# Kernel optimization log

Hardware: AMD Instinct MI355X
Metric: run time of the kernel (lower is better)

## Reference

```python
import jax, jax.numpy as jnp
import numpy as np

HEADS = 4
DIM_HEAD = 128

def setup_inputs() -> dict:
    key = jax.random.key(0)
    k1, k2, k3, k4 = jax.random.split(key, 4)
    scale = DIM_HEAD ** -0.5
    return {
        "fmap": jax.random.normal(k1, (16, 512, 32, 32), dtype=jnp.float32),
        "w_qkv": jax.random.normal(k2, (1536, 512), dtype=jnp.float32) * 0.02,
        "height": jax.random.normal(k3, (32, DIM_HEAD), dtype=jnp.float32) * scale,
        "width": jax.random.normal(k4, (32, DIM_HEAD), dtype=jnp.float32) * scale,
    }

def reference(fmap, w_qkv, height, width):
    b, c, h, w = fmap.shape
    scale = DIM_HEAD ** -0.5
    # 1x1 conv == channel GEMM: (b, 3*heads*dim_head, h, w)
    qkv = jnp.einsum('bchw,oc->bohw', fmap, w_qkv)
    # split into q,k,v and reshape to (b, heads, seq, dim_head)
    qkv = qkv.reshape(b, 3, HEADS, DIM_HEAD, h * w)
    q, k, v = (jnp.transpose(qkv[:, i], (0, 1, 3, 2)) for i in range(3))
    # content logits
    sim = jnp.einsum('bhid,bhjd->bhij', q, k) * scale
    # absolute positional bias: emb[(x,y)] = height[x] + width[y]
    emb = (height[:, None, :] + width[None, :, :]).reshape(h * w, DIM_HEAD)
    sim = sim + jnp.einsum('bhid,jd->bhij', q, emb) * scale
    attn = jax.nn.softmax(sim, axis=-1)
    out = jnp.einsum('bhij,bhjd->bhid', attn, v)  # (b, heads, seq, d)
    out = jnp.transpose(out, (0, 1, 3, 2)).reshape(b, HEADS * DIM_HEAD, h, w)
    return out
```

## Files before the change

### kernel.cpp

```cpp
#include <hip/hip_runtime.h>
#include <math.h>

#define HEADS 4
#define DIMH  128
#define NB    16
#define CIN   512
#define SEQ   1024
#define OTOT  1536
#define KQ    (CIN / 8)

typedef __attribute__((ext_vector_type(8)))  short bf16x8;
typedef __attribute__((ext_vector_type(4)))  short bf16x4;
typedef __attribute__((ext_vector_type(4)))  float f32x4;
typedef __attribute__((ext_vector_type(16))) float f32x16;

#define MFMA16(a,b,c) __builtin_amdgcn_mfma_f32_16x16x32_bf16(a,b,c,0,0,0)
#define MFMA32(a,b,c) __builtin_amdgcn_mfma_f32_32x32x16_bf16(a,b,c,0,0,0)

__device__ __forceinline__ short f2bf(float f) {
    unsigned u = __builtin_bit_cast(unsigned, f);
    u = (u + 0x7FFFu + ((u >> 16) & 1u)) >> 16;
    return (short)u;
}
__device__ __forceinline__ unsigned pk2(float lo, float hi) {
    return __builtin_amdgcn_perm(__builtin_bit_cast(unsigned, hi),
                                 __builtin_bit_cast(unsigned, lo), 0x07060302u);
}
union PF8 { unsigned u[4]; bf16x8 v; };

__device__ __forceinline__ void gll16(const short* g, short* l) {
    __builtin_amdgcn_global_load_lds(
        (const __attribute__((address_space(1))) unsigned*)g,
        (__attribute__((address_space(3))) unsigned*)l,
        16, 0, 0);
}

__global__ __launch_bounds__(256) void convert_all(const float* __restrict__ F,
                                                   const float* __restrict__ W,
                                                   short* __restrict__ FT2,
                                                   short* __restrict__ Wb2) {
    const int kq = blockIdx.y;
    if (blockIdx.z == NB) {
        const int o = blockIdx.x * 256 + threadIdx.x;
        float4 v0 = *(const float4*)&W[(size_t)o * CIN + kq * 8];
        float4 v1 = *(const float4*)&W[(size_t)o * CIN + kq * 8 + 4];
        bf16x8 pk = { f2bf(v0.x), f2bf(v0.y), f2bf(v0.z), f2bf(v0.w),
                      f2bf(v1.x), f2bf(v1.y), f2bf(v1.z), f2bf(v1.w) };
        *(bf16x8*)&Wb2[((size_t)kq * OTOT + o) * 8] = pk;
        return;
    }
    if (blockIdx.x >= 4) return;
    const int s = blockIdx.x * 256 + threadIdx.x;
    const int b = blockIdx.z;
    const float* src = F + ((size_t)b * CIN + kq * 8) * SEQ + s;
    float v[8];
    #pragma unroll
    for (int i = 0; i < 8; ++i) v[i] = src[(size_t)i * SEQ];
    bf16x8 pk = { f2bf(v[0]), f2bf(v[1]), f2bf(v[2]), f2bf(v[3]),
                  f2bf(v[4]), f2bf(v[5]), f2bf(v[6]), f2bf(v[7]) };
    *(bf16x8*)&FT2[(((size_t)b * KQ + kq) * SEQ + s) * 8] = pk;
}

__global__ __launch_bounds__(256, 3) void qkv_gemm(
    const short* __restrict__ Wb2, const short* __restrict__ FT2,
    const float* __restrict__ height, const float* __restrict__ width,
    short* __restrict__ Qo, short* __restrict__ Kfo, short* __restrict__ Vfo)
{
    __shared__ short As[2][4 * 128 * 8];
    __shared__ short Bs[2][4 * 128 * 8];

    const int L  = blockIdx.x;
    const int x8 = L & 7, m = L >> 3;
    const int g  = x8 + 8 * (m / 12);
    const int oy = m % 12;
    const int b  = g >> 3, sx = g & 7;
    const int o0 = oy * 128, s0 = sx * 128;

    const int t = threadIdx.x, l = t & 63, w = t >> 6;
    const int quad = l >> 4, ln = l & 15;
    const int wrow = (w >> 1) * 64, wcol = (w & 1) * 64;

#define STAGE(ks, buf) { \
    _Pragma("unroll") for (int r = 0; r < 4; ++r) { \
        const int task = r * 4 + w; \
        const int p = task >> 1, hf = task & 1; \
        if (p < 4) { \
            const short* gsrc = Wb2 + (((size_t)((ks) * 4 + p) * OTOT) + o0 + hf * 64 + l) * 8; \
            gll16(gsrc, &As[buf][(p * 128 + hf * 64) * 8]); \
        } else { \
            const short* gsrc = FT2 + ((((size_t)b * KQ + (ks) * 4 + (p - 4)) * SEQ) + s0 + hf * 64 + l) * 8; \
            gll16(gsrc, &Bs[buf][((p - 4) * 128 + hf * 64) * 8]); \
        } \
    } }

    f32x4 acc[4][4] = {};

    STAGE(0, 0);
    __syncthreads();

    for (int ks = 0; ks < 16; ++ks) {
        const int cb = ks & 1;
        if (ks < 15) STAGE(ks + 1, cb ^ 1);
        const short* Ab = &As[cb][0];
        const short* Bb = &Bs[cb][0];
        bf16x8 af[4], bfr[4];
        #pragma unroll
        for (int i = 0; i < 4; ++i)
            af[i]  = *(const bf16x8*)&Ab[((size_t)quad * 128 + wrow + i * 16 + ln) * 8];
        #pragma unroll
        for (int j = 0; j < 4; ++j)
            bfr[j] = *(const bf16x8*)&Bb[((size_t)quad * 128 + wcol + j * 16 + ln) * 8];
        #pragma unroll
        for (int i = 0; i < 4; ++i)
            #pragma unroll
            for (int j = 0; j < 4; ++j)
                acc[i][j] = MFMA16(af[i], bfr[j], acc[i][j]);
        __syncthreads();
    }

    const int sec = o0 >> 9;
    const int h   = (o0 >> 7) & 3;
    const size_t bh = (size_t)b * HEADS + h;

    if (sec == 0) {
        const float qs = 0.08838834764831845f * 1.4426950408889634f;
        #pragma unroll
        for (int ti = 0; ti < 4; ++ti) {
            int d = wrow + ti * 16 + quad * 4;
            #pragma unroll
            for (int tj = 0; tj < 4; ++tj) {
                int s = s0 + wcol + tj * 16 + ln;
                f32x4 a = acc[ti][tj];
                bf16x4 pk4 = { f2bf(a[0]*qs), f2bf(a[1]*qs), f2bf(a[2]*qs), f2bf(a[3]*qs) };
                *(bf16x4*)&Qo[(bh * SEQ + s) * DIMH + d] = pk4;
            }
        }
    } else if (sec == 1) {
        #pragma unroll
        for (int ti = 0; ti < 4; ++ti) {
            int d = wrow + ti * 16 + quad * 4;
            #pragma unroll
            for (int tj = 0; tj < 4; ++tj) {
                int s = s0 + wcol + tj * 16 + ln;
                float4 hv = *(const float4*)&height[(size_t)(s >> 5) * DIMH + d];
                float4 wv = *(const float4*)&width[(size_t)(s & 31) * DIMH + d];
                f32x4 a = acc[ti][tj];
                bf16x4 pk4 = { f2bf(a[0] + hv.x + wv.x), f2bf(a[1] + hv.y + wv.y),
                               f2bf(a[2] + hv.z + wv.z), f2bf(a[3] + hv.w + wv.w) };
                *(bf16x4*)&Kfo[(((size_t)bh * 16 + (d >> 3)) * SEQ + s) * 8 + (d & 7)] = pk4;
            }
        }
    } else {
        const int slot = ((ln >> 2) & 1) * 8 + (ln & 3) + ((ln >> 3) << 2);
        #pragma unroll
        for (int ti = 0; ti < 4; ++ti) {
            int d = wrow + ti * 16 + quad * 4;
            #pragma unroll
            for (int tj = 0; tj < 4; ++tj) {
                int s = s0 + wcol + tj * 16 + ln;
                size_t vb = (((size_t)bh * 64 + (s >> 4)) * DIMH) * 16 + slot;
                f32x4 a = acc[ti][tj];
                #pragma unroll
                for (int r = 0; r < 4; ++r)
                    Vfo[vb + (size_t)(d + r) * 16] = f2bf(a[r]);
            }
        }
    }
}

#define BQ 128
#define BJ 64
#define KSTR 136

#define ATTN_ITER(ti, DO_QK, DO_PRE, DO_BAR)                                        \
{                                                                                   \
    const int rd = (((ti) + 1) & 1) * (BJ * KSTR);                                  \
    const int wr = ((ti) & 1) * (BJ * KSTR);                                        \
    const short* vp0 = Vlane + (size_t)((ti) * 4) * (DIMH * 16);                    \
    bf16x8 vr[4][4];                                                                \
    _Pragma("unroll") for (int gi = 0; gi < 2; ++gi)                                \
      _Pragma("unroll") for (int dc = 0; dc < 4; ++dc)                              \
        vr[gi][dc] = *(const bf16x8*)(vp0 + (size_t)gi * (DIMH * 16) + dc * 32 * 16);\
    int4 kreg[4];                                                                   \
    if (DO_PRE) {                                                                   \
        _Pragma("unroll") for (int p = 0; p < 4; ++p)                               \
            kreg[p] = *(const int4*)(Kg + ((size_t)(p * 4 + w) * SEQ + ((ti) + 2) * BJ + l) * 8); \
    }                                                                               \
    PF8 pf[4];                                                                      \
    _Pragma("unroll") for (int g = 0; g < 4; ++g) {                                 \
        const f32x16& Sh = (g & 2) ? S1 : S0;                                       \
        const int kk = g & 1;                                                       \
        _Pragma("unroll") for (int mm = 0; mm < 4; ++mm) {                          \
            float ea = __builtin_amdgcn_exp2f(Sh[kk * 8 + 2 * mm]);                 \
            float eb = __builtin_amdgcn_exp2f(Sh[kk * 8 + 2 * mm + 1]);             \
            psum += ea + eb;                                                        \
            pf[g].u[mm] = pk2(ea, eb);                                              \
        }                                                                           \
    }                                                                               \
    _Pragma("unroll") for (int gi = 2; gi < 4; ++gi)                                \
      _Pragma("unroll") for (int dc = 0; dc < 4; ++dc)                              \
        vr[gi][dc] = *(const bf16x8*)(vp0 + (size_t)gi * (DIMH * 16) + dc * 32 * 16);\
    if (DO_QK) {                                                                    \
        S0 = (f32x16){}; S1 = (f32x16){};                                           \
        _Pragma("unroll") for (int kc = 0; kc < 8; ++kc) {                          \
            bf16x8 k0 = *(const bf16x8*)&Ks[rd + c31 * KSTR + kc * 16 + h * 8];     \
            bf16x8 k1 = *(const bf16x8*)&Ks[rd + (32 + c31) * KSTR + kc * 16 + h * 8]; \
            S0 = MFMA32(k0, qf[kc], S0);                                            \
            S1 = MFMA32(k1, qf[kc], S1);                                            \
        }                                                                           \
    }                                                                               \
    _Pragma("unroll") for (int g = 0; g < 4; ++g)                                   \
        _Pragma("unroll") for (int dc = 0; dc < 4; ++dc)                            \
            O[dc] = MFMA32(vr[g][dc], pf[g].v, O[dc]);                              \
    if (DO_PRE) {                                                                   \
        _Pragma("unroll") for (int p = 0; p < 4; ++p)                               \
            *(int4*)&Ks[wr + l * KSTR + (p * 4 + w) * 8] = kreg[p];                 \
    }                                                                               \
    if (DO_BAR) __syncthreads();                                                    \
}

__global__ __launch_bounds__(256, 2) void attn(
    const short* __restrict__ Q, const short* __restrict__ Kf,
    const short* __restrict__ Vf, float* __restrict__ out)
{
    __shared__ short Ks[2 * BJ * KSTR];

    const int t = threadIdx.x, l = t & 63, w = t >> 6;
    const int h = l >> 5, c31 = l & 31;

    const int L = blockIdx.x;
    const int x = L & 7, inner = L >> 3;
    const int bh = x * 8 + (inner >> 3);
    const int q0 = (inner & 7) * BQ;
    const size_t obase = (size_t)bh * DIMH * SEQ;

    bf16x8 qf[8];
    {
        const short* Qp = Q + ((size_t)bh * SEQ + (q0 + w * 32 + c31)) * DIMH + h * 8;
        #pragma unroll
        for (int kc = 0; kc < 8; ++kc)
            qf[kc] = *(const bf16x8*)(Qp + kc * 16);
    }

    const short* Kg = Kf + (size_t)bh * 16 * SEQ * 8;
    const short* Vlane = Vf + (size_t)bh * 64 * (DIMH * 16) + (c31 * 16 + h * 8);

    f32x16 O[4] = {};
    float psum = 0.f;

    {
        int4 k0[4], k1[4];
        #pragma unroll
        for (int p = 0; p < 4; ++p) {
            k0[p] = *(const int4*)(Kg + ((size_t)(p * 4 + w) * SEQ + l) * 8);
            k1[p] = *(const int4*)(Kg + ((size_t)(p * 4 + w) * SEQ + BJ + l) * 8);
        }
        #pragma unroll
        for (int p = 0; p < 4; ++p) {
            *(int4*)&Ks[l * KSTR + (p * 4 + w) * 8] = k0[p];
            *(int4*)&Ks[BJ * KSTR + l * KSTR + (p * 4 + w) * 8] = k1[p];
        }
    }
    __syncthreads();

    f32x16 S0 = {}, S1 = {};
    #pragma unroll
    for (int kc = 0; kc < 8; ++kc) {
        bf16x8 k0 = *(const bf16x8*)&Ks[c31 * KSTR + kc * 16 + h * 8];
        bf16x8 k1 = *(const bf16x8*)&Ks[(32 + c31) * KSTR + kc * 16 + h * 8];
        S0 = MFMA32(k0, qf[kc], S0);
        S1 = MFMA32(k1, qf[kc], S1);
    }
    __syncthreads();

    for (int p = 0; p < 7; ++p) {
        const int t0 = 2 * p;
        ATTN_ITER(t0,     true, true, true);
        ATTN_ITER(t0 + 1, true, true, true);
    }
    ATTN_ITER(14, true,  false, false);
    ATTN_ITER(15, false, false, false);

    psum += __shfl_xor(psum, 32);
    float linv = 1.0f / psum;

    #pragma unroll
    for (int dc = 0; dc < 4; ++dc)
        #pragma unroll
        for (int r = 0; r < 16; ++r) {
            int d = dc * 32 + (r & 3) + 8 * (r >> 2) + 4 * h;
            out[obase + (size_t)d * SEQ + q0 + w * 32 + c31] = O[dc][r] * linv;
        }
}

extern "C" void kernel_launch(void* const* d_in, const int* in_sizes, int n_in,
                              void* d_out, int out_size, void* d_ws, size_t ws_size,
                              hipStream_t stream) {
    const float* fmap   = (const float*)d_in[0];
    const float* w_qkv  = (const float*)d_in[1];
    const float* height = (const float*)d_in[2];
    const float* width  = (const float*)d_in[3];
    float* outp = (float*)d_out;

    const size_t n_ft  = (size_t)NB * SEQ * CIN;
    const size_t n_w   = (size_t)OTOT * CIN;
    const size_t n_qkv = (size_t)NB * HEADS * SEQ * DIMH;

    short* FT2 = (short*)d_ws;
    short* Wb2 = FT2 + n_ft;
    short* Qb  = Wb2 + n_w;
    short* Kfb = Qb + n_qkv;
    short* Vfb = Kfb + n_qkv;

    convert_all<<<dim3(6, KQ, NB + 1), 256, 0, stream>>>(fmap, w_qkv, FT2, Wb2);
    qkv_gemm<<<dim3(8 * 12 * NB), 256, 0, stream>>>(
        Wb2, FT2, height, width, Qb, Kfb, Vfb);
    attn<<<dim3(NB * HEADS * (SEQ / BQ)), 256, 0, stream>>>(Qb, Kfb, Vfb, outp);
}
```

Baseline: 171.4 us.

## Load K fragments directly from global into registers, drop LDS staging and barriers

K tiles are no longer staged through shared memory with double buffering and block barriers. Each wave instead loads its K MFMA operands straight from global memory into registers, one tile ahead, and MFMA sections are wrapped in s_setprio to raise wave priority. This removes the LDS round trip and the __syncthreads in every iteration. In exchange, every wave fetches K redundantly (four times more global/L2 traffic), register pressure rises with 16 extra bf16x8 fragments, and the loop is now fully unrolled.

```diff
diff --git a/kernel.cpp b/kernel.cpp
--- a/kernel.cpp
+++ b/kernel.cpp
@@ -170,22 +170,21 @@
 
 #define BQ 128
 #define BJ 64
-#define KSTR 136
-
-#define ATTN_ITER(ti, DO_QK, DO_PRE, DO_BAR)                                        \
+
+#define KLOAD(tile) { \
+    const short* kp = Kg + ((size_t)h * SEQ + (tile) * BJ + c31) * 8; \
+    _Pragma("unroll") for (int kc = 0; kc < 8; ++kc) { \
+        ka0[kc] = *(const bf16x8*)(kp + (size_t)(kc * 2) * SEQ * 8); \
+        ka1[kc] = *(const bf16x8*)(kp + ((size_t)(kc * 2) * SEQ + 32) * 8); \
+    } }
+
+#define ATTN_ITER(ti, DO_QK, DO_PRE)                                                \
 {                                                                                   \
-    const int rd = (((ti) + 1) & 1) * (BJ * KSTR);                                  \
-    const int wr = ((ti) & 1) * (BJ * KSTR);                                        \
     const short* vp0 = Vlane + (size_t)((ti) * 4) * (DIMH * 16);                    \
     bf16x8 vr[4][4];                                                                \
     _Pragma("unroll") for (int gi = 0; gi < 2; ++gi)                                \
       _Pragma("unroll") for (int dc = 0; dc < 4; ++dc)                              \
         vr[gi][dc] = *(const bf16x8*)(vp0 + (size_t)gi * (DIMH * 16) + dc * 32 * 16);\
-    int4 kreg[4];                                                                   \
-    if (DO_PRE) {                                                                   \
-        _Pragma("unroll") for (int p = 0; p < 4; ++p)                               \
-            kreg[p] = *(const int4*)(Kg + ((size_t)(p * 4 + w) * SEQ + ((ti) + 2) * BJ + l) * 8); \
-    }                                                                               \
     PF8 pf[4];                                                                      \
     _Pragma("unroll") for (int g = 0; g < 4; ++g) {                                 \
         const f32x16& Sh = (g & 2) ? S1 : S0;                                       \
@@ -197,34 +196,30 @@
             pf[g].u[mm] = pk2(ea, eb);                                              \
         }                                                                           \
     }                                                                               \
+    if (DO_QK) {                                                                    \
+        S0 = (f32x16){}; S1 = (f32x16){};                                           \
+        __builtin_amdgcn_s_setprio(1);                                              \
+        _Pragma("unroll") for (int kc = 0; kc < 8; ++kc) {                          \
+            S0 = MFMA32(ka0[kc], qf[kc], S0);                                       \
+            S1 = MFMA32(ka1[kc], qf[kc], S1);                                       \
+        }                                                                           \
+        __builtin_amdgcn_s_setprio(0);                                              \
+    }                                                                               \
+    if (DO_PRE) KLOAD((ti) + 2);                                                    \
     _Pragma("unroll") for (int gi = 2; gi < 4; ++gi)                                \
       _Pragma("unroll") for (int dc = 0; dc < 4; ++dc)                              \
         vr[gi][dc] = *(const bf16x8*)(vp0 + (size_t)gi * (DIMH * 16) + dc * 32 * 16);\
-    if (DO_QK) {                                                                    \
-        S0 = (f32x16){}; S1 = (f32x16){};                                           \
-        _Pragma("unroll") for (int kc = 0; kc < 8; ++kc) {                          \
-            bf16x8 k0 = *(const bf16x8*)&Ks[rd + c31 * KSTR + kc * 16 + h * 8];     \
-            bf16x8 k1 = *(const bf16x8*)&Ks[rd + (32 + c31) * KSTR + kc * 16 + h * 8]; \
-            S0 = MFMA32(k0, qf[kc], S0);                                            \
-            S1 = MFMA32(k1, qf[kc], S1);                                            \
-        }                                                                           \
-    }                                                                               \
+    __builtin_amdgcn_s_setprio(1);                                                  \
     _Pragma("unroll") for (int g = 0; g < 4; ++g)                                   \
         _Pragma("unroll") for (int dc = 0; dc < 4; ++dc)                            \
             O[dc] = MFMA32(vr[g][dc], pf[g].v, O[dc]);                              \
-    if (DO_PRE) {                                                                   \
-        _Pragma("unroll") for (int p = 0; p < 4; ++p)                               \
-            *(int4*)&Ks[wr + l * KSTR + (p * 4 + w) * 8] = kreg[p];                 \
-    }                                                                               \
-    if (DO_BAR) __syncthreads();                                                    \
+    __builtin_amdgcn_s_setprio(0);                                                  \
 }
 
 __global__ __launch_bounds__(256, 2) void attn(
     const short* __restrict__ Q, const short* __restrict__ Kf,
     const short* __restrict__ Vf, float* __restrict__ out)
 {
-    __shared__ short Ks[2 * BJ * KSTR];
-
     const int t = threadIdx.x, l = t & 63, w = t >> 6;
     const int h = l >> 5, c31 = l & 31;
 
@@ -247,39 +242,23 @@
 
     f32x16 O[4] = {};
     float psum = 0.f;
-
-    {
-        int4 k0[4], k1[4];
-        #pragma unroll
-        for (int p = 0; p < 4; ++p) {
-            k0[p] = *(const int4*)(Kg + ((size_t)(p * 4 + w) * SEQ + l) * 8);
-            k1[p] = *(const int4*)(Kg + ((size_t)(p * 4 + w) * SEQ + BJ + l) * 8);
-        }
-        #pragma unroll
-        for (int p = 0; p < 4; ++p) {
-            *(int4*)&Ks[l * KSTR + (p * 4 + w) * 8] = k0[p];
-            *(int4*)&Ks[BJ * KSTR + l * KSTR + (p * 4 + w) * 8] = k1[p];
-        }
-    }
-    __syncthreads();
+    bf16x8 ka0[8], ka1[8];
 
     f32x16 S0 = {}, S1 = {};
+    KLOAD(0);
     #pragma unroll
     for (int kc = 0; kc < 8; ++kc) {
-        bf16x8 k0 = *(const bf16x8*)&Ks[c31 * KSTR + kc * 16 + h * 8];
-        bf16x8 k1 = *(const bf16x8*)&Ks[(32 + c31) * KSTR + kc * 16 + h * 8];
-        S0 = MFMA32(k0, qf[kc], S0);
-        S1 = MFMA32(k1, qf[kc], S1);
-    }
-    __syncthreads();
-
-    for (int p = 0; p < 7; ++p) {
-        const int t0 = 2 * p;
-        ATTN_ITER(t0,     true, true, true);
-        ATTN_ITER(t0 + 1, true, true, true);
-    }
-    ATTN_ITER(14, true,  false, false);
-    ATTN_ITER(15, false, false, false);
+        S0 = MFMA32(ka0[kc], qf[kc], S0);
+        S1 = MFMA32(ka1[kc], qf[kc], S1);
+    }
+    KLOAD(1);
+
+    #pragma unroll
+    for (int ti = 0; ti < 14; ++ti) {
+        ATTN_ITER(ti, true, true);
+    }
+    ATTN_ITER(14, true,  false);
+    ATTN_ITER(15, false, false);
 
     psum += __shfl_xor(psum, 32);
     float linv = 1.0f / psum;
```

Measured after the change: 259.8 us. 51.6% more time.

## Split attention key range across two wave groups per block with LDS reduction

Applied to the files above, without the earlier changes.

The attention block grows from 4 to 8 waves. Each group of 4 waves handles half of the key sequence with its own double-buffered K tile in shared memory. At the end, group 1 writes its partial O accumulators and row sums to LDS, and group 0 combines them before normalising and storing. This doubles the parallelism per query tile and halves the serial loop length, meant to improve latency hiding with 512 blocks on 256 CUs. The cost is extra LDS, a cross-group reduction and tighter register limits from launch_bounds(512,4).

```diff
diff --git a/kernel.cpp b/kernel.cpp
--- a/kernel.cpp
+++ b/kernel.cpp
@@ -171,12 +171,14 @@
 #define BQ 128
 #define BJ 64
 #define KSTR 136
+#define HALF 8
 
 #define ATTN_ITER(ti, DO_QK, DO_PRE, DO_BAR)                                        \
 {                                                                                   \
-    const int rd = (((ti) + 1) & 1) * (BJ * KSTR);                                  \
-    const int wr = ((ti) & 1) * (BJ * KSTR);                                        \
-    const short* vp0 = Vlane + (size_t)((ti) * 4) * (DIMH * 16);                    \
+    const int AT = tbase + (ti);                                                    \
+    const int rd = gbase + (((ti) + 1) & 1) * (BJ * KSTR);                          \
+    const int wr = gbase + ((ti) & 1) * (BJ * KSTR);                                \
+    const short* vp0 = Vlane + (size_t)(AT * 4) * (DIMH * 16);                      \
     bf16x8 vr[4][4];                                                                \
     _Pragma("unroll") for (int gi = 0; gi < 2; ++gi)                                \
       _Pragma("unroll") for (int dc = 0; dc < 4; ++dc)                              \
@@ -184,17 +186,17 @@
     int4 kreg[4];                                                                   \
     if (DO_PRE) {                                                                   \
         _Pragma("unroll") for (int p = 0; p < 4; ++p)                               \
-            kreg[p] = *(const int4*)(Kg + ((size_t)(p * 4 + w) * SEQ + ((ti) + 2) * BJ + l) * 8); \
+            kreg[p] = *(const int4*)(Kg + ((size_t)(p * 4 + w) * SEQ + (AT + 2) * BJ + l) * 8); \
     }                                                                               \
     PF8 pf[4];                                                                      \
-    _Pragma("unroll") for (int g = 0; g < 4; ++g) {                                 \
-        const f32x16& Sh = (g & 2) ? S1 : S0;                                       \
-        const int kk = g & 1;                                                       \
+    _Pragma("unroll") for (int gq = 0; gq < 4; ++gq) {                              \
+        const f32x16& Sh = (gq & 2) ? S1 : S0;                                      \
+        const int kk = gq & 1;                                                      \
         _Pragma("unroll") for (int mm = 0; mm < 4; ++mm) {                          \
             float ea = __builtin_amdgcn_exp2f(Sh[kk * 8 + 2 * mm]);                 \
             float eb = __builtin_amdgcn_exp2f(Sh[kk * 8 + 2 * mm + 1]);             \
             psum += ea + eb;                                                        \
-            pf[g].u[mm] = pk2(ea, eb);                                              \
+            pf[gq].u[mm] = pk2(ea, eb);                                             \
         }                                                                           \
     }                                                                               \
     _Pragma("unroll") for (int gi = 2; gi < 4; ++gi)                                \
@@ -209,9 +211,9 @@
             S1 = MFMA32(k1, qf[kc], S1);                                            \
         }                                                                           \
     }                                                                               \
-    _Pragma("unroll") for (int g = 0; g < 4; ++g)                                   \
+    _Pragma("unroll") for (int gq = 0; gq < 4; ++gq)                                \
         _Pragma("unroll") for (int dc = 0; dc < 4; ++dc)                            \
-            O[dc] = MFMA32(vr[g][dc], pf[g].v, O[dc]);                              \
+            O[dc] = MFMA32(vr[gq][dc], pf[gq].v, O[dc]);                            \
     if (DO_PRE) {                                                                   \
         _Pragma("unroll") for (int p = 0; p < 4; ++p)                               \
             *(int4*)&Ks[wr + l * KSTR + (p * 4 + w) * 8] = kreg[p];                 \
@@ -219,14 +221,17 @@
     if (DO_BAR) __syncthreads();                                                    \
 }
 
-__global__ __launch_bounds__(256, 2) void attn(
+__global__ __launch_bounds__(512, 4) void attn(
     const short* __restrict__ Q, const short* __restrict__ Kf,
     const short* __restrict__ Vf, float* __restrict__ out)
 {
-    __shared__ short Ks[2 * BJ * KSTR];
-
-    const int t = threadIdx.x, l = t & 63, w = t >> 6;
+    __shared__ short Ks[4 * BJ * KSTR];
+
+    const int t = threadIdx.x, l = t & 63, w8 = t >> 6;
+    const int g = w8 >> 2, w = w8 & 3;
     const int h = l >> 5, c31 = l & 31;
+    const int tbase = g * HALF;
+    const int gbase = g * 2 * (BJ * KSTR);
 
     const int L = blockIdx.x;
     const int x = L & 7, inner = L >> 3;
@@ -252,13 +257,13 @@
         int4 k0[4], k1[4];
         #pragma unroll
         for (int p = 0; p < 4; ++p) {
-            k0[p] = *(const int4*)(Kg + ((size_t)(p * 4 + w) * SEQ + l) * 8);
-            k1[p] = *(const int4*)(Kg + ((size_t)(p * 4 + w) * SEQ + BJ + l) * 8);
+            k0[p] = *(const int4*)(Kg + ((size_t)(p * 4 + w) * SEQ + tbase * BJ + l) * 8);
+            k1[p] = *(const int4*)(Kg + ((size_t)(p * 4 + w) * SEQ + (tbase + 1) * BJ + l) * 8);
         }
         #pragma unroll
         for (int p = 0; p < 4; ++p) {
-            *(int4*)&Ks[l * KSTR + (p * 4 + w) * 8] = k0[p];
-            *(int4*)&Ks[BJ * KSTR + l * KSTR + (p * 4 + w) * 8] = k1[p];
+            *(int4*)&Ks[gbase + l * KSTR + (p * 4 + w) * 8] = k0[p];
+            *(int4*)&Ks[gbase + BJ * KSTR + l * KSTR + (p * 4 + w) * 8] = k1[p];
         }
     }
     __syncthreads();
@@ -266,31 +271,48 @@
     f32x16 S0 = {}, S1 = {};
     #pragma unroll
     for (int kc = 0; kc < 8; ++kc) {
-        bf16x8 k0 = *(const bf16x8*)&Ks[c31 * KSTR + kc * 16 + h * 8];
-        bf16x8 k1 = *(const bf16x8*)&Ks[(32 + c31) * KSTR + kc * 16 + h * 8];
+        bf16x8 k0 = *(const bf16x8*)&Ks[gbase + c31 * KSTR + kc * 16 + h * 8];
+        bf16x8 k1 = *(const bf16x8*)&Ks[gbase + (32 + c31) * KSTR + kc * 16 + h * 8];
         S0 = MFMA32(k0, qf[kc], S0);
         S1 = MFMA32(k1, qf[kc], S1);
     }
     __syncthreads();
 
-    for (int p = 0; p < 7; ++p) {
+    for (int p = 0; p < 3; ++p) {
         const int t0 = 2 * p;
         ATTN_ITER(t0,     true, true, true);
         ATTN_ITER(t0 + 1, true, true, true);
     }
-    ATTN_ITER(14, true,  false, false);
-    ATTN_ITER(15, false, false, false);
+    ATTN_ITER(6, true,  false, false);
+    ATTN_ITER(7, false, false, false);
 
     psum += __shfl_xor(psum, 32);
-    float linv = 1.0f / psum;
-
-    #pragma unroll
-    for (int dc = 0; dc < 4; ++dc)
-        #pragma unroll
-        for (int r = 0; r < 16; ++r) {
-            int d = dc * 32 + (r & 3) + 8 * (r >> 2) + 4 * h;
-            out[obase + (size_t)d * SEQ + q0 + w * 32 + c31] = O[dc][r] * linv;
-        }
+
+    __syncthreads();
+    float* xb = (float*)Ks;
+    const int xslot = (w * 64 + l) * 68;
+    if (g == 1) {
+        #pragma unroll
+        for (int dc = 0; dc < 4; ++dc)
+            #pragma unroll
+            for (int r4 = 0; r4 < 4; ++r4)
+                *(f32x4*)&xb[xslot + dc * 16 + r4 * 4] =
+                    (f32x4){ O[dc][r4 * 4 + 0], O[dc][r4 * 4 + 1],
+                             O[dc][r4 * 4 + 2], O[dc][r4 * 4 + 3] };
+        xb[xslot + 64] = psum;
+    }
+    __syncthreads();
+    if (g == 0) {
+        float linv = 1.0f / (psum + xb[xslot + 64]);
+        #pragma unroll
+        for (int dc = 0; dc < 4; ++dc)
+            #pragma unroll
+            for (int r = 0; r < 16; ++r) {
+                float v = O[dc][r] + xb[xslot + dc * 16 + r];
+                int d = dc * 32 + (r & 3) + 8 * (r >> 2) + 4 * h;
+                out[obase + (size_t)d * SEQ + q0 + w * 32 + c31] = v * linv;
+            }
+    }
 }
 
 extern "C" void kernel_launch(void* const* d_in, const int* in_sizes, int n_in,
@@ -315,5 +337,5 @@
     convert_all<<<dim3(6, KQ, NB + 1), 256, 0, stream>>>(fmap, w_qkv, FT2, Wb2);
     qkv_gemm<<<dim3(8 * 12 * NB), 256, 0, stream>>>(
         Wb2, FT2, height, width, Qb, Kfb, Vfb);
-    attn<<<dim3(NB * HEADS * (SEQ / BQ)), 256, 0, stream>>>(Qb, Kfb, Vfb, outp);
-}
+    attn<<<dim3(NB * HEADS * (SEQ / BQ)), 512, 0, stream>>>(Qb, Kfb, Vfb, outp);
+}
```

Measured after the change: 616.8 us. 3.6x slower.
